# Kernel tuning notes

Hardware: AMD Instinct MI355X
Metric: run time of the kernel (lower is better)

## Reference

```python
import jax, jax.numpy as jnp
import numpy as np

N_NODES = 50000
N_EDGES = 800000
IN_DIM = 128
HIDDEN = 128
NUM_CLASSES = 64
NEG_SLOPE = 0.2


def setup_inputs() -> dict:
    key = jax.random.key(0)
    ks = jax.random.split(key, 12)
    x = jax.random.normal(ks[0], (N_NODES, IN_DIM), dtype=jnp.float32)
    src = jax.random.randint(ks[1], (N_EDGES,), 0, N_NODES, dtype=jnp.int64)
    dst = jax.random.randint(ks[2], (N_EDGES,), 0, N_NODES, dtype=jnp.int64)
    def glorot(k, shape):
        fan_in, fan_out = shape[0], shape[-1]
        s = jnp.sqrt(2.0 / (fan_in + fan_out)).astype(jnp.float32)
        return jax.random.normal(k, shape, dtype=jnp.float32) * s
    return {
        "x": x, "src": src, "dst": dst,
        # GATConv params (1 head, no bias, no residual)
        "W_gat": glorot(ks[3], (IN_DIM, HIDDEN)),
        "attn_l": glorot(ks[4], (HIDDEN,)),
        "attn_r": glorot(ks[5], (HIDDEN,)),
        # GraphConv params (norm='none', bias=True)
        "W1": glorot(ks[6], (HIDDEN, HIDDEN)),
        "b1": jnp.zeros((HIDDEN,), dtype=jnp.float32),
        "W2": glorot(ks[7], (HIDDEN, HIDDEN)),
        "b2": jnp.zeros((HIDDEN,), dtype=jnp.float32),
        "Wc": glorot(ks[8], (HIDDEN, NUM_CLASSES)),
        "bc": jnp.zeros((NUM_CLASSES,), dtype=jnp.float32),
    }


def reference(x, src, dst, W_gat, attn_l, attn_r, W1, b1, W2, b2, Wc, bc):
    N = x.shape[0]
    # --- GATConv, single head, eval mode (dropout=0) ---
    h = x @ W_gat                      # (N, H)
    el = h @ attn_l                    # (N,)
    er = h @ attn_r                    # (N,)
    e = jax.nn.leaky_relu(el[src] + er[dst], negative_slope=NEG_SLOPE)  # (E,)
    # edge softmax over incoming edges of each dst node
    emax = jax.ops.segment_max(e, dst, num_segments=N)
    ee = jnp.exp(e - emax[dst])
    esum = jax.ops.segment_sum(ee, dst, num_segments=N)
    alpha = ee / esum[dst]             # (E,) attention = reused edge weights
    h1 = jax.ops.segment_sum(h[src] * alpha[:, None], dst, num_segments=N)
    h1 = jax.nn.elu(h1)                # GATConv activation

    # --- GraphConv (norm='none') with edge_weight = alpha ---
    def gconv(hin, W, b):
        hp = hin @ W                                   # project (order is math-equivalent)
        agg = jax.ops.segment_sum(hp[src] * alpha[:, None], dst, num_segments=N)
        return agg + b

    h2 = gconv(h1, W1, b1)
    h3 = gconv(h2, W2, b2)
    logits = gconv(h3, Wc, bc)         # (N, num_classes)
    return logits
```

## Files before the change

### kernel.cpp

```cpp
#include <hip/hip_runtime.h>
#include <hip/hip_fp16.h>
#include <math.h>

#define N_NODES 50000
#define N_EDGES 800000
#define PAD_EDGES (N_EDGES + 16 * N_NODES)

typedef _Float16 half8 __attribute__((ext_vector_type(8)));
typedef float floatx16 __attribute__((ext_vector_type(16)));

#define NPREPA_BLK 129
#define NPREPP_BLK 33
#define NEDGE_BLK 3125
#define NSCAN_BLK 196

__global__ __launch_bounds__(256) void k1_prep_hist(const int* __restrict__ dst,
                                                    const float* __restrict__ Wg,
                                                    const float* __restrict__ W1,
                                                    const float* __restrict__ W2,
                                                    const float* __restrict__ b1,
                                                    int* __restrict__ deg,
                                                    int* __restrict__ rank,
                                                    __half* __restrict__ Wg_hl,
                                                    float* __restrict__ W12,
                                                    float* __restrict__ c12) {
  int b = blockIdx.x;
  if (b >= NPREPA_BLK) {
    int e = (b - NPREPA_BLK) * 256 + threadIdx.x;
    if (e < N_EDGES) rank[e] = atomicAdd(&deg[dst[e]], 1);
    return;
  }
  int e = b * 256 + threadIdx.x;
  if (e < 16384) {
    _Float16* o = (_Float16*)Wg_hl;
    int k = e >> 7, n = e & 127;
    float w = Wg[k * 128 + n];
    _Float16 hi = (_Float16)w;
    float lo = w - (float)hi;
    int oi = (((k >> 3) * 128 + n) << 3) | (k & 7);
    o[oi] = hi;
    o[16384 + oi] = (_Float16)lo;
  } else if (e < 32768) {
    int local = e - 16384;
    int k = local >> 7, n = local & 127;
    float acc = 0.f;
    for (int j = 0; j < 128; ++j) acc = fmaf(W1[k * 128 + j], W2[j * 128 + n], acc);
    W12[k * 128 + n] = acc;
  } else if (e < 32896) {
    int n = e - 32768;
    float acc = 0.f;
    for (int j = 0; j < 128; ++j) acc = fmaf(b1[j], W2[j * 128 + n], acc);
    c12[n] = acc;
  }
}

__global__ __launch_bounds__(256) void scan1_k(const int* __restrict__ deg,
                                               int* __restrict__ offs,
                                               int* __restrict__ bsum, int N) {
  __shared__ int s[256];
  int t = threadIdx.x;
  int i = blockIdx.x * 256 + t;
  int v = 0;
  if (i < N) {
    int d = deg[i];
    v = (d + 15) & ~15;
    if (v < 16) v = 16;
  }
  s[t] = v;
  __syncthreads();
  for (int o = 1; o < 256; o <<= 1) {
    int add = (t >= o) ? s[t - o] : 0;
    __syncthreads();
    s[t] += add;
    __syncthreads();
  }
  if (i < N) offs[i] = s[t] - v;
  if (t == 255) bsum[blockIdx.x] = s[255];
}

__global__ __launch_bounds__(256) void scan3_k(int* __restrict__ offs,
                                               const int* __restrict__ deg,
                                               const int* __restrict__ bsum,
                                               int N, int nb) {
  __shared__ int s[256];
  int t = threadIdx.x;
  int b = blockIdx.x;
  s[t] = (t < nb && t < b) ? bsum[t] : 0;
  __syncthreads();
  for (int o = 128; o; o >>= 1) {
    if (t < o) s[t] += s[t + o];
    __syncthreads();
  }
  int base = s[0];
  int i = b * 256 + t;
  if (i < N) {
    int o = offs[i] + base;
    offs[i] = o;
    if (i == N - 1) {
      int d = deg[i];
      int pd = (d + 15) & ~15;
      if (pd < 16) pd = 16;
      offs[N] = o + pd;
    }
  }
}

__global__ __launch_bounds__(256) void k4_prepP_scatter(const int* __restrict__ src,
                                                        const int* __restrict__ dst,
                                                        const int* __restrict__ offs,
                                                        const int* __restrict__ rank,
                                                        int* __restrict__ csr_src,
                                                        const float* __restrict__ W12,
                                                        const float* __restrict__ c12,
                                                        const float* __restrict__ Wc,
                                                        const float* __restrict__ b2,
                                                        __half* __restrict__ WPhl,
                                                        float* __restrict__ c1,
                                                        float* __restrict__ c2) {
  int b = blockIdx.x;
  if (b >= NPREPP_BLK) {
    int e = (b - NPREPP_BLK) * 256 + threadIdx.x;
    if (e < N_EDGES) csr_src[offs[dst[e]] + rank[e]] = src[e];
    return;
  }
  int e = b * 256 + threadIdx.x;
  _Float16* o = (_Float16*)WPhl;
  if (e < 8192) {
    int k = e >> 6, n = e & 63;
    float acc = 0.f;
    for (int j = 0; j < 128; ++j) acc = fmaf(W12[k * 128 + j], Wc[j * 64 + n], acc);
    _Float16 hi = (_Float16)acc;
    float lo = acc - (float)hi;
    int oi = (((k >> 3) * 64 + n) << 3) | (k & 7);
    o[oi] = hi;
    o[8192 + oi] = (_Float16)lo;
  } else if (e < 8256) {
    int n = e - 8192;
    float acc = 0.f;
    for (int j = 0; j < 128; ++j) acc = fmaf(c12[j], Wc[j * 64 + n], acc);
    c1[n] = acc;
  } else if (e < 8320) {
    int n = e - 8256;
    float acc = 0.f;
    for (int j = 0; j < 128; ++j) acc = fmaf(b2[j], Wc[j * 64 + n], acc);
    c2[n] = acc;
  }
}

template <int NCOL, bool A16, bool ELR>
__global__ __launch_bounds__(256) void mgemm_k(const void* __restrict__ Ap,
                                               const __half* __restrict__ Whl,
                                               __half* __restrict__ C16, int M,
                                               const float* __restrict__ al,
                                               const float* __restrict__ ar,
                                               float2* __restrict__ el2,
                                               float* __restrict__ er,
                                               const int* __restrict__ deg) {
  __shared__ __half Al[16][129][8];
  const int tid  = threadIdx.x;
  const int row0 = blockIdx.x * 128;
  const int lane = tid & 63;
  const int lane31 = lane & 31;
  const int q = lane >> 5;
  const int r = tid >> 6;

  if (A16) {
    const uint4* A8 = (const uint4*)Ap;
    #pragma unroll
    for (int i = 0; i < 8; ++i) {
      int idx = tid + i * 256;
      int row = idx >> 4, c = idx & 15;
      int grow = row0 + row;
      uint4 v = make_uint4(0u, 0u, 0u, 0u);
      if (grow < M) v = A8[grow * 16 + c];
      *reinterpret_cast<uint4*>(&Al[c][row][0]) = v;
    }
  } else {
    const float4* A4 = (const float4*)Ap;
    #pragma unroll
    for (int i = 0; i < 8; ++i) {
      int idx = tid + i * 256;
      int row = idx >> 4, c = idx & 15;
      int grow = row0 + row;
      half8 hv = {};
      if (grow < M) {
        float4 a0 = A4[grow * 32 + c * 2];
        float4 a1 = A4[grow * 32 + c * 2 + 1];
        hv[0] = (_Float16)a0.x; hv[1] = (_Float16)a0.y;
        hv[2] = (_Float16)a0.z; hv[3] = (_Float16)a0.w;
        hv[4] = (_Float16)a1.x; hv[5] = (_Float16)a1.y;
        hv[6] = (_Float16)a1.z; hv[7] = (_Float16)a1.w;
      }
      *reinterpret_cast<half8*>(&Al[c][row][0]) = hv;
    }
  }
  __syncthreads();

  half8 afr[8];
  #pragma unroll
  for (int s = 0; s < 8; ++s)
    afr[s] = *reinterpret_cast<const half8*>(&Al[2 * s + q][r * 32 + lane31][0]);

  const half8* B8 = reinterpret_cast<const half8*>(Whl);
  const int KN8 = 16 * NCOL;

  float elp[16], erp[16];
  if (ELR) {
    #pragma unroll
    for (int i = 0; i < 16; ++i) { elp[i] = 0.f; erp[i] = 0.f; }
  }

  #pragma unroll
  for (int tc = 0; tc < NCOL / 32; ++tc) {
    floatx16 acc = {};
    int nbase = tc * 32 + lane31;
    #pragma unroll
    for (int s = 0; s < 8; ++s) {
      int ci = (2 * s + q) * NCOL + nbase;
      half8 bl = B8[KN8 + ci];
      half8 bh = B8[ci];
      acc = __builtin_amdgcn_mfma_f32_32x32x16_f16(afr[s], bl, acc, 0, 0, 0);
      acc = __builtin_amdgcn_mfma_f32_32x32x16_f16(afr[s], bh, acc, 0, 0, 0);
    }
    if (ELR) {
      float alv = al[nbase], arv = ar[nbase];
      #pragma unroll
      for (int i = 0; i < 16; ++i) {
        elp[i] = fmaf(acc[i], alv, elp[i]);
        erp[i] = fmaf(acc[i], arv, erp[i]);
      }
    }
    #pragma unroll
    for (int i = 0; i < 16; ++i) {
      int rl = (i & 3) + 8 * (i >> 2) + 4 * q;
      int grow = row0 + r * 32 + rl;
      if (grow < M) C16[grow * NCOL + nbase] = __float2half(acc[i]);
    }
  }

  if (ELR) {
    #pragma unroll
    for (int off = 1; off <= 16; off <<= 1) {
      #pragma unroll
      for (int i = 0; i < 16; ++i) {
        elp[i] += __shfl_xor(elp[i], off);
        erp[i] += __shfl_xor(erp[i], off);
      }
    }
    if (lane31 == 0) {
      #pragma unroll
      for (int i = 0; i < 16; ++i) {
        int rl = (i & 3) + 8 * (i >> 2) + 4 * q;
        int grow = row0 + r * 32 + rl;
        if (grow < M) {
          er[grow] = erp[i];
          el2[grow] = make_float2(elp[i], (deg[grow] > 0) ? 1.f : 0.f);
        }
      }
    }
  }
}

__device__ inline void fma8(float2 acc[4], uint4 u, float a) {
  __half2* h = reinterpret_cast<__half2*>(&u);
  #pragma unroll
  for (int j = 0; j < 4; ++j) {
    float2 f = __half22float2(h[j]);
    acc[j].x = fmaf(a, f.x, acc[j].x);
    acc[j].y = fmaf(a, f.y, acc[j].y);
  }
}

__global__ __launch_bounds__(256) void aggsm_k(const int* __restrict__ offs,
                                               const int* __restrict__ deg,
                                               const int* __restrict__ csr_src,
                                               const float2* __restrict__ el2,
                                               const float* __restrict__ er,
                                               int2* __restrict__ meta,
                                               float* __restrict__ t,
                                               const __half* __restrict__ hp,
                                               __half* __restrict__ out, int N) {
  __shared__ int2 lmeta[4][64];
  int wv   = threadIdx.x >> 6;
  int w    = (blockIdx.x * 256 + threadIdx.x) >> 6;
  int lane = threadIdx.x & 63;
  if (w >= N) return;
  int o0   = offs[w];
  int pcnt = offs[w + 1] - o0;
  int cnt  = deg[w];
  int q  = lane >> 4;
  int fl = lane & 15;
  const uint4* hpq = reinterpret_cast<const uint4*>(hp);

  if (cnt <= 64) {
    bool valid = lane < cnt;
    float erv = er[w];
    int s = 0;
    float ev = -3.4e38f, flag = 0.f;
    if (valid) {
      s = csr_src[o0 + lane];
      float2 e2 = el2[s];
      float e0 = e2.x + erv;
      ev = (e0 >= 0.f) ? e0 : 0.2f * e0;
      flag = e2.y;
    }
    float m = ev;
    #pragma unroll
    for (int off = 32; off; off >>= 1) m = fmaxf(m, __shfl_xor(m, off));
    float ee = valid ? __expf(ev - m) : 0.f;
    float sum = ee, tp = ee * flag;
    #pragma unroll
    for (int off = 32; off; off >>= 1) {
      sum += __shfl_xor(sum, off);
      tp  += __shfl_xor(tp, off);
    }
    float inv = (cnt > 0) ? 1.f / sum : 0.f;
    int2 mm = make_int2(0, 0);
    if (valid) mm = make_int2(s * 16, __float_as_int(ee * inv));
    if (lane < pcnt) meta[o0 + lane] = mm;
    lmeta[wv][lane] = mm;
    if (lane == 0) t[w] = tp * inv;
  } else {
    float erv = er[w];
    float m = -3.4e38f;
    for (int i = lane; i < cnt; i += 64) {
      int s = csr_src[o0 + i];
      float2 e2 = el2[s];
      float ev = e2.x + erv;
      ev = (ev >= 0.f) ? ev : 0.2f * ev;
      m = fmaxf(m, ev);
    }
    #pragma unroll
    for (int off = 32; off; off >>= 1) m = fmaxf(m, __shfl_xor(m, off));
    float sum = 0.f, tacc = 0.f;
    int myS = 0; float myE = 0.f;
    for (int i = lane; i < cnt; i += 64) {
      int s = csr_src[o0 + i];
      float2 e2 = el2[s];
      float ev = e2.x + erv;
      ev = (ev >= 0.f) ? ev : 0.2f * ev;
      float ee = __expf(ev - m);
      meta[o0 + i] = make_int2(s * 16, __float_as_int(ee));
      sum += ee;
      tacc += ee * e2.y;
      if (i == lane) { myS = s; myE = ee; }
    }
    #pragma unroll
    for (int off = 32; off; off >>= 1) {
      sum  += __shfl_xor(sum, off);
      tacc += __shfl_xor(tacc, off);
    }
    float inv = 1.f / sum;
    if (lane == 0) t[w] = tacc * inv;
    for (int i = lane; i < cnt; i += 64) {
      int2 mm = meta[o0 + i];
      meta[o0 + i] = make_int2(mm.x, __float_as_int(__int_as_float(mm.y) * inv));
    }
    for (int i = cnt + lane; i < pcnt; i += 64) meta[o0 + i] = make_int2(0, 0);
    lmeta[wv][lane] = make_int2(myS * 16, __float_as_int(myE * inv));
  }

  float2 acc0[4] = {}, acc1[4] = {};
  int pc = pcnt < 64 ? pcnt : 64;
  int2 mA = lmeta[wv][q], mB = lmeta[wv][4 + q];
  for (int base = 8; base < pc; base += 8) {
    int2 nA = lmeta[wv][base + q], nB = lmeta[wv][base + 4 + q];
    uint4 vA = hpq[mA.x + fl], vB = hpq[mB.x + fl];
    fma8(acc0, vA, __int_as_float(mA.y));
    fma8(acc1, vB, __int_as_float(mB.y));
    mA = nA; mB = nB;
  }
  {
    uint4 vA = hpq[mA.x + fl], vB = hpq[mB.x + fl];
    fma8(acc0, vA, __int_as_float(mA.y));
    fma8(acc1, vB, __int_as_float(mB.y));
  }
  for (int p = o0 + 64 + q; p < o0 + pcnt; p += 4) {
    int2 mm = meta[p];
    fma8(acc0, hpq[mm.x + fl], __int_as_float(mm.y));
  }
  #pragma unroll
  for (int j = 0; j < 4; ++j) { acc0[j].x += acc1[j].x; acc0[j].y += acc1[j].y; }
  #pragma unroll
  for (int off = 16; off <= 32; off <<= 1) {
    #pragma unroll
    for (int j = 0; j < 4; ++j) {
      acc0[j].x += __shfl_xor(acc0[j].x, off);
      acc0[j].y += __shfl_xor(acc0[j].y, off);
    }
  }
  if (q == 0) {
    float o8[8];
    #pragma unroll
    for (int j = 0; j < 4; ++j) { o8[2 * j] = acc0[j].x; o8[2 * j + 1] = acc0[j].y; }
    #pragma unroll
    for (int j = 0; j < 8; ++j) o8[j] = (o8[j] > 0.f) ? o8[j] : (__expf(o8[j]) - 1.f);
    __half2 p0 = __floats2half2_rn(o8[0], o8[1]);
    __half2 p1 = __floats2half2_rn(o8[2], o8[3]);
    __half2 p2 = __floats2half2_rn(o8[4], o8[5]);
    __half2 p3 = __floats2half2_rn(o8[6], o8[7]);
    uint4 pk;
    pk.x = *reinterpret_cast<unsigned*>(&p0);
    pk.y = *reinterpret_cast<unsigned*>(&p1);
    pk.z = *reinterpret_cast<unsigned*>(&p2);
    pk.w = *reinterpret_cast<unsigned*>(&p3);
    *reinterpret_cast<uint4*>(&out[w * 128 + fl * 8]) = pk;
  }
}

template <bool FINAL>
__global__ __launch_bounds__(256) void agg64v_k(const int* __restrict__ offs,
                                                const int2* __restrict__ meta,
                                                const __half* __restrict__ zp,
                                                const float* __restrict__ t,
                                                const int* __restrict__ deg,
                                                const float* __restrict__ c1,
                                                const float* __restrict__ c2,
                                                const float* __restrict__ bc,
                                                void* __restrict__ outp, int N) {
  int w    = (blockIdx.x * 256 + threadIdx.x) >> 6;
  int lane = threadIdx.x & 63;
  if (w >= N) return;
  int o0 = offs[w], o1 = offs[w + 1];
  int o   = lane >> 3;
  int fl  = lane & 7;
  const uint4* hpq = reinterpret_cast<const uint4*>(zp);

  float2 acc0[4] = {}, acc1[4] = {};
  int p = o0 + o;
  int2 mA = meta[p], mB = meta[p + 8];
  for (; p + 16 < o1; p += 16) {
    int2 nA = meta[p + 16], nB = meta[p + 24];
    uint4 vA = hpq[(mA.x >> 1) + fl];
    uint4 vB = hpq[(mB.x >> 1) + fl];
    fma8(acc0, vA, __int_as_float(mA.y));
    fma8(acc1, vB, __int_as_float(mB.y));
    mA = nA; mB = nB;
  }
  {
    uint4 vA = hpq[(mA.x >> 1) + fl];
    uint4 vB = hpq[(mB.x >> 1) + fl];
    fma8(acc0, vA, __int_as_float(mA.y));
    fma8(acc1, vB, __int_as_float(mB.y));
  }
  #pragma unroll
  for (int j = 0; j < 4; ++j) { acc0[j].x += acc1[j].x; acc0[j].y += acc1[j].y; }
  #pragma unroll
  for (int off = 8; off <= 32; off <<= 1) {
    #pragma unroll
    for (int j = 0; j < 4; ++j) {
      acc0[j].x += __shfl_xor(acc0[j].x, off);
      acc0[j].y += __shfl_xor(acc0[j].y, off);
    }
  }
  if (o == 0) {
    float o8[8];
    #pragma unroll
    for (int j = 0; j < 4; ++j) { o8[2 * j] = acc0[j].x; o8[2 * j + 1] = acc0[j].y; }
    if (FINAL) {
      float tw = t[w];
      float dw = (deg[w] > 0) ? 1.f : 0.f;
      float4 a0 = reinterpret_cast<const float4*>(c1)[fl * 2];
      float4 a1 = reinterpret_cast<const float4*>(c1)[fl * 2 + 1];
      float4 d0 = reinterpret_cast<const float4*>(c2)[fl * 2];
      float4 d1 = reinterpret_cast<const float4*>(c2)[fl * 2 + 1];
      float4 b0 = reinterpret_cast<const float4*>(bc)[fl * 2];
      float4 b1v = reinterpret_cast<const float4*>(bc)[fl * 2 + 1];
      o8[0] += tw * a0.x + dw * d0.x + b0.x;
      o8[1] += tw * a0.y + dw * d0.y + b0.y;
      o8[2] += tw * a0.z + dw * d0.z + b0.z;
      o8[3] += tw * a0.w + dw * d0.w + b0.w;
      o8[4] += tw * a1.x + dw * d1.x + b1v.x;
      o8[5] += tw * a1.y + dw * d1.y + b1v.y;
      o8[6] += tw * a1.z + dw * d1.z + b1v.z;
      o8[7] += tw * a1.w + dw * d1.w + b1v.w;
      float4* of = reinterpret_cast<float4*>(outp);
      of[w * 16 + fl * 2]     = make_float4(o8[0], o8[1], o8[2], o8[3]);
      of[w * 16 + fl * 2 + 1] = make_float4(o8[4], o8[5], o8[6], o8[7]);
    } else {
      __half2 p0 = __floats2half2_rn(o8[0], o8[1]);
      __half2 p1 = __floats2half2_rn(o8[2], o8[3]);
      __half2 p2 = __floats2half2_rn(o8[4], o8[5]);
      __half2 p3 = __floats2half2_rn(o8[6], o8[7]);
      uint4 pk;
      pk.x = *reinterpret_cast<unsigned*>(&p0);
      pk.y = *reinterpret_cast<unsigned*>(&p1);
      pk.z = *reinterpret_cast<unsigned*>(&p2);
      pk.w = *reinterpret_cast<unsigned*>(&p3);
      reinterpret_cast<uint4*>(outp)[w * 8 + fl] = pk;
    }
  }
}

extern "C" void kernel_launch(void* const* d_in, const int* in_sizes, int n_in,
                              void* d_out, int out_size, void* d_ws, size_t ws_size,
                              hipStream_t stream) {
  const float* x      = (const float*)d_in[0];
  const int*   src    = (const int*)d_in[1];
  const int*   dst    = (const int*)d_in[2];
  const float* W_gat  = (const float*)d_in[3];
  const float* attn_l = (const float*)d_in[4];
  const float* attn_r = (const float*)d_in[5];
  const float* W1     = (const float*)d_in[6];
  const float* b1     = (const float*)d_in[7];
  const float* W2     = (const float*)d_in[8];
  const float* b2     = (const float*)d_in[9];
  const float* Wc     = (const float*)d_in[10];
  const float* bc     = (const float*)d_in[11];
  float* out = (float*)d_out;

  char* ws = (char*)d_ws;
  size_t off = 0;
  auto walloc = [&](size_t bytes) -> void* {
    void* p = ws + off;
    off += (bytes + 255) & ~size_t(255);
    return p;
  };
  __half* P16     = (__half*)walloc((size_t)N_NODES * 128 * 2);
  __half* F16     = (__half*)walloc((size_t)N_NODES * 128 * 2);
  float*  er      = (float*)walloc((size_t)N_NODES * 4);
  float2* el2     = (float2*)walloc((size_t)N_NODES * 8);
  float*  tbuf    = (float*)walloc((size_t)N_NODES * 4);
  int*    deg     = (int*)walloc((size_t)N_NODES * 4);
  int*    offs    = (int*)walloc((size_t)(N_NODES + 1) * 4);
  int*    rank    = (int*)walloc((size_t)N_EDGES * 4);
  int*    csr_src = (int*)walloc((size_t)PAD_EDGES * 4);
  int2*   meta    = (int2*)walloc((size_t)PAD_EDGES * 8);
  int*    bsum    = (int*)walloc(1024);
  __half* Wg_hl   = (__half*)walloc((size_t)32768 * 2);
  __half* WP_hl   = (__half*)walloc((size_t)16384 * 2);
  float*  W12     = (float*)walloc((size_t)16384 * 4);
  float*  c12     = (float*)walloc((size_t)128 * 4);
  float*  c1      = (float*)walloc((size_t)64 * 4);
  float*  c2      = (float*)walloc((size_t)64 * 4);

  hipMemsetAsync(deg, 0, (size_t)N_NODES * 4, stream);

  const dim3 blk(256);
  const int nwave_blocks = (N_NODES + 3) / 4;
  const int ngemm_blocks = (N_NODES + 127) / 128;

  k1_prep_hist<<<dim3(NPREPA_BLK + NEDGE_BLK), blk, 0, stream>>>(
      dst, W_gat, W1, W2, b1, deg, rank, Wg_hl, W12, c12);
  scan1_k<<<dim3(NSCAN_BLK), blk, 0, stream>>>(deg, offs, bsum, N_NODES);
  scan3_k<<<dim3(NSCAN_BLK), blk, 0, stream>>>(offs, deg, bsum, N_NODES, NSCAN_BLK);
  k4_prepP_scatter<<<dim3(NPREPP_BLK + NEDGE_BLK), blk, 0, stream>>>(
      src, dst, offs, rank, csr_src, W12, c12, Wc, b2, WP_hl, c1, c2);

  mgemm_k<128, false, true><<<dim3(ngemm_blocks), blk, 0, stream>>>(
      x, Wg_hl, P16, N_NODES, attn_l, attn_r, el2, er, deg);

  aggsm_k<<<dim3(nwave_blocks), blk, 0, stream>>>(offs, deg, csr_src, el2, er, meta, tbuf, P16, F16, N_NODES);
  mgemm_k<64, true, false><<<dim3(ngemm_blocks), blk, 0, stream>>>(
      F16, WP_hl, P16, N_NODES, nullptr, nullptr, nullptr, nullptr, nullptr);
  agg64v_k<false><<<dim3(nwave_blocks), blk, 0, stream>>>(offs, meta, P16, nullptr, nullptr, nullptr, nullptr, nullptr, F16, N_NODES);
  agg64v_k<false><<<dim3(nwave_blocks), blk, 0, stream>>>(offs, meta, F16, nullptr, nullptr, nullptr, nullptr, nullptr, P16, N_NODES);
  agg64v_k<true><<<dim3(nwave_blocks), blk, 0, stream>>>(offs, meta, P16, tbuf, deg, c1, c2, bc, out, N_NODES);
}
```

Measured before the change: 271.5 us.

## Fuse scan passes with decoupled lookback, shrink segment padding, specialize short-degree loops

Measured after the change: 282.0 us. +3.8%, slower.

```diff
diff --git a/kernel.cpp b/kernel.cpp
--- a/kernel.cpp
+++ b/kernel.cpp
@@ -4,7 +4,7 @@
 
 #define N_NODES 50000
 #define N_EDGES 800000
-#define PAD_EDGES (N_EDGES + 16 * N_NODES)
+#define PAD_EDGES (N_EDGES + 8 * N_NODES)
 
 typedef _Float16 half8 __attribute__((ext_vector_type(8)));
 typedef float floatx16 __attribute__((ext_vector_type(16)));
@@ -54,17 +54,51 @@
   }
 }
 
-__global__ __launch_bounds__(256) void scan1_k(const int* __restrict__ deg,
+__global__ __launch_bounds__(256) void scanP_k(const int* __restrict__ deg,
                                                int* __restrict__ offs,
-                                               int* __restrict__ bsum, int N) {
+                                               int* __restrict__ bsum,
+                                               int* __restrict__ bflag,
+                                               const float* __restrict__ W12,
+                                               const float* __restrict__ c12,
+                                               const float* __restrict__ Wc,
+                                               const float* __restrict__ b2,
+                                               __half* __restrict__ WPhl,
+                                               float* __restrict__ c1,
+                                               float* __restrict__ c2, int N) {
+  int b = blockIdx.x;
+  int t = threadIdx.x;
+  if (b >= NSCAN_BLK) {
+    int e = (b - NSCAN_BLK) * 256 + t;
+    _Float16* o = (_Float16*)WPhl;
+    if (e < 8192) {
+      int k = e >> 6, n = e & 63;
+      float acc = 0.f;
+      for (int j = 0; j < 128; ++j) acc = fmaf(W12[k * 128 + j], Wc[j * 64 + n], acc);
+      _Float16 hi = (_Float16)acc;
+      float lo = acc - (float)hi;
+      int oi = (((k >> 3) * 64 + n) << 3) | (k & 7);
+      o[oi] = hi;
+      o[8192 + oi] = (_Float16)lo;
+    } else if (e < 8256) {
+      int n = e - 8192;
+      float acc = 0.f;
+      for (int j = 0; j < 128; ++j) acc = fmaf(c12[j], Wc[j * 64 + n], acc);
+      c1[n] = acc;
+    } else if (e < 8320) {
+      int n = e - 8256;
+      float acc = 0.f;
+      for (int j = 0; j < 128; ++j) acc = fmaf(b2[j], Wc[j * 64 + n], acc);
+      c2[n] = acc;
+    }
+    return;
+  }
   __shared__ int s[256];
-  int t = threadIdx.x;
-  int i = blockIdx.x * 256 + t;
+  int i = b * 256 + t;
   int v = 0;
   if (i < N) {
     int d = deg[i];
-    v = (d + 15) & ~15;
-    if (v < 16) v = 16;
+    v = (d + 7) & ~7;
+    if (v < 8) v = 8;
   }
   s[t] = v;
   __syncthreads();
@@ -74,77 +108,44 @@
     s[t] += add;
     __syncthreads();
   }
-  if (i < N) offs[i] = s[t] - v;
-  if (t == 255) bsum[blockIdx.x] = s[255];
-}
-
-__global__ __launch_bounds__(256) void scan3_k(int* __restrict__ offs,
-                                               const int* __restrict__ deg,
-                                               const int* __restrict__ bsum,
-                                               int N, int nb) {
-  __shared__ int s[256];
-  int t = threadIdx.x;
-  int b = blockIdx.x;
-  s[t] = (t < nb && t < b) ? bsum[t] : 0;
+  int loc = s[t] - v;
+  if (t == 255) {
+    bsum[b] = s[255];
+    __hip_atomic_store(&bflag[b], 1, __ATOMIC_RELEASE, __HIP_MEMORY_SCOPE_AGENT);
+  }
+  int contrib = 0;
+  if (t < b) {
+    while (!__hip_atomic_load(&bflag[t], __ATOMIC_ACQUIRE, __HIP_MEMORY_SCOPE_AGENT))
+      __builtin_amdgcn_s_sleep(2);
+    contrib = bsum[t];
+  }
+  __syncthreads();
+  s[t] = contrib;
   __syncthreads();
   for (int o = 128; o; o >>= 1) {
     if (t < o) s[t] += s[t + o];
     __syncthreads();
   }
   int base = s[0];
-  int i = b * 256 + t;
   if (i < N) {
-    int o = offs[i] + base;
+    int o = loc + base;
     offs[i] = o;
     if (i == N - 1) {
       int d = deg[i];
-      int pd = (d + 15) & ~15;
-      if (pd < 16) pd = 16;
+      int pd = (d + 7) & ~7;
+      if (pd < 8) pd = 8;
       offs[N] = o + pd;
     }
   }
 }
 
-__global__ __launch_bounds__(256) void k4_prepP_scatter(const int* __restrict__ src,
-                                                        const int* __restrict__ dst,
-                                                        const int* __restrict__ offs,
-                                                        const int* __restrict__ rank,
-                                                        int* __restrict__ csr_src,
-                                                        const float* __restrict__ W12,
-                                                        const float* __restrict__ c12,
-                                                        const float* __restrict__ Wc,
-                                                        const float* __restrict__ b2,
-                                                        __half* __restrict__ WPhl,
-                                                        float* __restrict__ c1,
-                                                        float* __restrict__ c2) {
-  int b = blockIdx.x;
-  if (b >= NPREPP_BLK) {
-    int e = (b - NPREPP_BLK) * 256 + threadIdx.x;
-    if (e < N_EDGES) csr_src[offs[dst[e]] + rank[e]] = src[e];
-    return;
-  }
-  int e = b * 256 + threadIdx.x;
-  _Float16* o = (_Float16*)WPhl;
-  if (e < 8192) {
-    int k = e >> 6, n = e & 63;
-    float acc = 0.f;
-    for (int j = 0; j < 128; ++j) acc = fmaf(W12[k * 128 + j], Wc[j * 64 + n], acc);
-    _Float16 hi = (_Float16)acc;
-    float lo = acc - (float)hi;
-    int oi = (((k >> 3) * 64 + n) << 3) | (k & 7);
-    o[oi] = hi;
-    o[8192 + oi] = (_Float16)lo;
-  } else if (e < 8256) {
-    int n = e - 8192;
-    float acc = 0.f;
-    for (int j = 0; j < 128; ++j) acc = fmaf(c12[j], Wc[j * 64 + n], acc);
-    c1[n] = acc;
-  } else if (e < 8320) {
-    int n = e - 8256;
-    float acc = 0.f;
-    for (int j = 0; j < 128; ++j) acc = fmaf(b2[j], Wc[j * 64 + n], acc);
-    c2[n] = acc;
-  }
+__global__ __launch_bounds__(256) void scat_k(const int* __restrict__ src,
+                                              const int* __restrict__ dst,
+                                              const int* __restrict__ offs,
+                                              const int* __restrict__ rank,
+                                              int* __restrict__ csr_src) {
+  int e = blockIdx.x * 256 + threadIdx.x;
+  if (e < N_EDGES) csr_src[offs[dst[e]] + rank[e]] = src[e];
 }
 
 template <int NCOL, bool A16, bool ELR>
@@ -362,15 +363,43 @@
 
   float2 acc0[4] = {}, acc1[4] = {};
   int pc = pcnt < 64 ? pcnt : 64;
-  int2 mA = lmeta[wv][q], mB = lmeta[wv][4 + q];
-  for (int base = 8; base < pc; base += 8) {
-    int2 nA = lmeta[wv][base + q], nB = lmeta[wv][base + 4 + q];
+  int n8 = pc >> 3;
+  if (n8 == 1) {
+    int2 mA = lmeta[wv][q], mB = lmeta[wv][4 + q];
     uint4 vA = hpq[mA.x + fl], vB = hpq[mB.x + fl];
     fma8(acc0, vA, __int_as_float(mA.y));
     fma8(acc1, vB, __int_as_float(mB.y));
-    mA = nA; mB = nB;
-  }
-  {
+  } else if (n8 == 2) {
+    int2 mA0 = lmeta[wv][q],     mB0 = lmeta[wv][4 + q];
+    int2 mA1 = lmeta[wv][8 + q], mB1 = lmeta[wv][12 + q];
+    uint4 vA0 = hpq[mA0.x + fl], vB0 = hpq[mB0.x + fl];
+    uint4 vA1 = hpq[mA1.x + fl], vB1 = hpq[mB1.x + fl];
+    fma8(acc0, vA0, __int_as_float(mA0.y));
+    fma8(acc1, vB0, __int_as_float(mB0.y));
+    fma8(acc0, vA1, __int_as_float(mA1.y));
+    fma8(acc1, vB1, __int_as_float(mB1.y));
+  } else if (n8 == 3) {
+    int2 mA0 = lmeta[wv][q],      mB0 = lmeta[wv][4 + q];
+    int2 mA1 = lmeta[wv][8 + q],  mB1 = lmeta[wv][12 + q];
+    int2 mA2 = lmeta[wv][16 + q], mB2 = lmeta[wv][20 + q];
+    uint4 vA0 = hpq[mA0.x + fl], vB0 = hpq[mB0.x + fl];
+    uint4 vA1 = hpq[mA1.x + fl], vB1 = hpq[mB1.x + fl];
+    uint4 vA2 = hpq[mA2.x + fl], vB2 = hpq[mB2.x + fl];
+    fma8(acc0, vA0, __int_as_float(mA0.y));
+    fma8(acc1, vB0, __int_as_float(mB0.y));
+    fma8(acc0, vA1, __int_as_float(mA1.y));
+    fma8(acc1, vB1, __int_as_float(mB1.y));
+    fma8(acc0, vA2, __int_as_float(mA2.y));
+    fma8(acc1, vB2, __int_as_float(mB2.y));
+  } else {
+    int2 mA = lmeta[wv][q], mB = lmeta[wv][4 + q];
+    for (int base = 8; base < pc; base += 8) {
+      int2 nA = lmeta[wv][base + q], nB = lmeta[wv][base + 4 + q];
+      uint4 vA = hpq[mA.x + fl], vB = hpq[mB.x + fl];
+      fma8(acc0, vA, __int_as_float(mA.y));
+      fma8(acc1, vB, __int_as_float(mB.y));
+      mA = nA; mB = nB;
+    }
     uint4 vA = hpq[mA.x + fl], vB = hpq[mB.x + fl];
     fma8(acc0, vA, __int_as_float(mA.y));
     fma8(acc1, vB, __int_as_float(mB.y));
@@ -428,20 +457,39 @@
 
   float2 acc0[4] = {}, acc1[4] = {};
   int p = o0 + o;
-  int2 mA = meta[p], mB = meta[p + 8];
-  for (; p + 16 < o1; p += 16) {
-    int2 nA = meta[p + 16], nB = meta[p + 24];
+  int n8 = (o1 - o0) >> 3;
+  if (n8 == 1) {
+    int2 m = meta[p];
+    uint4 v = hpq[(m.x >> 1) + fl];
+    fma8(acc0, v, __int_as_float(m.y));
+  } else if (n8 == 2) {
+    int2 mA = meta[p], mB = meta[p + 8];
     uint4 vA = hpq[(mA.x >> 1) + fl];
     uint4 vB = hpq[(mB.x >> 1) + fl];
     fma8(acc0, vA, __int_as_float(mA.y));
     fma8(acc1, vB, __int_as_float(mB.y));
-    mA = nA; mB = nB;
-  }
-  {
+  } else if (n8 == 3) {
+    int2 mA = meta[p], mB = meta[p + 8], mC = meta[p + 16];
     uint4 vA = hpq[(mA.x >> 1) + fl];
     uint4 vB = hpq[(mB.x >> 1) + fl];
+    uint4 vC = hpq[(mC.x >> 1) + fl];
     fma8(acc0, vA, __int_as_float(mA.y));
     fma8(acc1, vB, __int_as_float(mB.y));
+    fma8(acc0, vC, __int_as_float(mC.y));
+  } else {
+    if (n8 & 1) {
+      int2 m = meta[p];
+      uint4 v = hpq[(m.x >> 1) + fl];
+      fma8(acc0, v, __int_as_float(m.y));
+      p += 8;
+    }
+    for (; p < o1; p += 16) {
+      int2 mA = meta[p], mB = meta[p + 8];
+      uint4 vA = hpq[(mA.x >> 1) + fl];
+      uint4 vB = hpq[(mB.x >> 1) + fl];
+      fma8(acc0, vA, __int_as_float(mA.y));
+      fma8(acc1, vB, __int_as_float(mB.y));
+    }
   }
   #pragma unroll
   for (int j = 0; j < 4; ++j) { acc0[j].x += acc1[j].x; acc0[j].y += acc1[j].y; }
@@ -521,7 +569,8 @@
   float*  er      = (float*)walloc((size_t)N_NODES * 4);
   float2* el2     = (float2*)walloc((size_t)N_NODES * 8);
   float*  tbuf    = (float*)walloc((size_t)N_NODES * 4);
-  int*    deg     = (int*)walloc((size_t)N_NODES * 4);
+  int*    deg     = (int*)walloc((size_t)N_NODES * 4 + 1024);
+  int*    bflag   = deg + N_NODES;
   int*    offs    = (int*)walloc((size_t)(N_NODES + 1) * 4);
   int*    rank    = (int*)walloc((size_t)N_EDGES * 4);
   int*    csr_src = (int*)walloc((size_t)PAD_EDGES * 4);
@@ -534,7 +583,7 @@
   float*  c1      = (float*)walloc((size_t)64 * 4);
   float*  c2      = (float*)walloc((size_t)64 * 4);
 
-  hipMemsetAsync(deg, 0, (size_t)N_NODES * 4, stream);
+  hipMemsetAsync(deg, 0, (size_t)N_NODES * 4 + 1024, stream);
 
   const dim3 blk(256);
   const int nwave_blocks = (N_NODES + 3) / 4;
@@ -542,10 +591,9 @@
 
   k1_prep_hist<<<dim3(NPREPA_BLK + NEDGE_BLK), blk, 0, stream>>>(
       dst, W_gat, W1, W2, b1, deg, rank, Wg_hl, W12, c12);
-  scan1_k<<<dim3(NSCAN_BLK), blk, 0, stream>>>(deg, offs, bsum, N_NODES);
-  scan3_k<<<dim3(NSCAN_BLK), blk, 0, stream>>>(offs, deg, bsum, N_NODES, NSCAN_BLK);
-  k4_prepP_scatter<<<dim3(NPREPP_BLK + NEDGE_BLK), blk, 0, stream>>>(
-      src, dst, offs, rank, csr_src, W12, c12, Wc, b2, WP_hl, c1, c2);
+  scanP_k<<<dim3(NSCAN_BLK + NPREPP_BLK), blk, 0, stream>>>(
+      deg, offs, bsum, bflag, W12, c12, Wc, b2, WP_hl, c1, c2, N_NODES);
+  scat_k<<<dim3(NEDGE_BLK), blk, 0, stream>>>(src, dst, offs, rank, csr_src);
 
   mgemm_k<128, false, true><<<dim3(ngemm_blocks), blk, 0, stream>>>(
       x, Wg_hl, P16, N_NODES, attn_l, attn_r, el2, er, deg);
```

## Fuse first GEMM into scan kernel and replace stored edge ranks with atomic cursors

Applied to the files above, without the earlier changes.

Result: slower. 294.7 us (+8.5%).

```diff
diff --git a/kernel.cpp b/kernel.cpp
--- a/kernel.cpp
+++ b/kernel.cpp
@@ -13,6 +13,7 @@
 #define NPREPP_BLK 33
 #define NEDGE_BLK 3125
 #define NSCAN_BLK 196
+#define NGEMM_BLK 391
 
 __global__ __launch_bounds__(256) void k1_prep_hist(const int* __restrict__ dst,
                                                     const float* __restrict__ Wg,
@@ -20,14 +21,13 @@
                                                     const float* __restrict__ W2,
                                                     const float* __restrict__ b1,
                                                     int* __restrict__ deg,
-                                                    int* __restrict__ rank,
                                                     __half* __restrict__ Wg_hl,
                                                     float* __restrict__ W12,
                                                     float* __restrict__ c12) {
   int b = blockIdx.x;
   if (b >= NPREPA_BLK) {
     int e = (b - NPREPA_BLK) * 256 + threadIdx.x;
-    if (e < N_EDGES) rank[e] = atomicAdd(&deg[dst[e]], 1);
+    if (e < N_EDGES) atomicAdd(&deg[dst[e]], 1);
     return;
   }
   int e = b * 256 + threadIdx.x;
@@ -54,17 +54,144 @@
   }
 }
 
-__global__ __launch_bounds__(256) void scan1_k(const int* __restrict__ deg,
-                                               int* __restrict__ offs,
-                                               int* __restrict__ bsum, int N) {
+template <int NCOL, bool A16, bool ELR>
+__device__ __forceinline__ void mgemm_body(int bid, const void* __restrict__ Ap,
+                                           const __half* __restrict__ Whl,
+                                           __half* __restrict__ C16, int M,
+                                           const float* __restrict__ al,
+                                           const float* __restrict__ ar,
+                                           float* __restrict__ el2x,
+                                           float* __restrict__ er) {
+  __shared__ __half Al[16][129][8];
+  const int tid  = threadIdx.x;
+  const int row0 = bid * 128;
+  const int lane = tid & 63;
+  const int lane31 = lane & 31;
+  const int q = lane >> 5;
+  const int r = tid >> 6;
+
+  if (A16) {
+    const uint4* A8 = (const uint4*)Ap;
+    #pragma unroll
+    for (int i = 0; i < 8; ++i) {
+      int idx = tid + i * 256;
+      int row = idx >> 4, c = idx & 15;
+      int grow = row0 + row;
+      uint4 v = make_uint4(0u, 0u, 0u, 0u);
+      if (grow < M) v = A8[grow * 16 + c];
+      *reinterpret_cast<uint4*>(&Al[c][row][0]) = v;
+    }
+  } else {
+    const float4* A4 = (const float4*)Ap;
+    #pragma unroll
+    for (int i = 0; i < 8; ++i) {
+      int idx = tid + i * 256;
+      int row = idx >> 4, c = idx & 15;
+      int grow = row0 + row;
+      half8 hv = {};
+      if (grow < M) {
+        float4 a0 = A4[grow * 32 + c * 2];
+        float4 a1 = A4[grow * 32 + c * 2 + 1];
+        hv[0] = (_Float16)a0.x; hv[1] = (_Float16)a0.y;
+        hv[2] = (_Float16)a0.z; hv[3] = (_Float16)a0.w;
+        hv[4] = (_Float16)a1.x; hv[5] = (_Float16)a1.y;
+        hv[6] = (_Float16)a1.z; hv[7] = (_Float16)a1.w;
+      }
+      *reinterpret_cast<half8*>(&Al[c][row][0]) = hv;
+    }
+  }
+  __syncthreads();
+
+  half8 afr[8];
+  #pragma unroll
+  for (int s = 0; s < 8; ++s)
+    afr[s] = *reinterpret_cast<const half8*>(&Al[2 * s + q][r * 32 + lane31][0]);
+
+  const half8* B8 = reinterpret_cast<const half8*>(Whl);
+  const int KN8 = 16 * NCOL;
+
+  float elp[16], erp[16];
+  if (ELR) {
+    #pragma unroll
+    for (int i = 0; i < 16; ++i) { elp[i] = 0.f; erp[i] = 0.f; }
+  }
+
+  #pragma unroll
+  for (int tc = 0; tc < NCOL / 32; ++tc) {
+    floatx16 acc = {};
+    int nbase = tc * 32 + lane31;
+    #pragma unroll
+    for (int s = 0; s < 8; ++s) {
+      int ci = (2 * s + q) * NCOL + nbase;
+      half8 bl = B8[KN8 + ci];
+      half8 bh = B8[ci];
+      acc = __builtin_amdgcn_mfma_f32_32x32x16_f16(afr[s], bl, acc, 0, 0, 0);
+      acc = __builtin_amdgcn_mfma_f32_32x32x16_f16(afr[s], bh, acc, 0, 0, 0);
+    }
+    if (ELR) {
+      float alv = al[nbase], arv = ar[nbase];
+      #pragma unroll
+      for (int i = 0; i < 16; ++i) {
+        elp[i] = fmaf(acc[i], alv, elp[i]);
+        erp[i] = fmaf(acc[i], arv, erp[i]);
+      }
+    }
+    #pragma unroll
+    for (int i = 0; i < 16; ++i) {
+      int rl = (i & 3) + 8 * (i >> 2) + 4 * q;
+      int grow = row0 + r * 32 + rl;
+      if (grow < M) C16[grow * NCOL + nbase] = __float2half(acc[i]);
+    }
+  }
+
+  if (ELR) {
+    #pragma unroll
+    for (int off = 1; off <= 16; off <<= 1) {
+      #pragma unroll
+      for (int i = 0; i < 16; ++i) {
+        elp[i] += __shfl_xor(elp[i], off);
+        erp[i] += __shfl_xor(erp[i], off);
+      }
+    }
+    if (lane31 == 0) {
+      #pragma unroll
+      for (int i = 0; i < 16; ++i) {
+        int rl = (i & 3) + 8 * (i >> 2) + 4 * q;
+        int grow = row0 + r * 32 + rl;
+        if (grow < M) {
+          er[grow] = erp[i];
+          el2x[2 * grow] = elp[i];
+        }
+      }
+    }
+  }
+}
+
+__global__ __launch_bounds__(256) void k2_scan_mgemm(const int* __restrict__ deg,
+                                                     int* __restrict__ offs,
+                                                     int* __restrict__ bsum,
+                                                     float2* __restrict__ el2,
+                                                     const float* __restrict__ x,
+                                                     const __half* __restrict__ Wg_hl,
+                                                     __half* __restrict__ P16,
+                                                     const float* __restrict__ al,
+                                                     const float* __restrict__ ar,
+                                                     float* __restrict__ er, int N) {
+  int b = blockIdx.x;
+  if (b >= NSCAN_BLK) {
+    mgemm_body<128, false, true>(b - NSCAN_BLK, x, Wg_hl, P16, N, al, ar,
+                                 reinterpret_cast<float*>(el2), er);
+    return;
+  }
   __shared__ int s[256];
   int t = threadIdx.x;
-  int i = blockIdx.x * 256 + t;
+  int i = b * 256 + t;
   int v = 0;
   if (i < N) {
     int d = deg[i];
     v = (d + 15) & ~15;
     if (v < 16) v = 16;
+    reinterpret_cast<float*>(el2)[2 * i + 1] = (d > 0) ? 1.f : 0.f;
   }
   s[t] = v;
   __syncthreads();
@@ -75,7 +202,7 @@
     __syncthreads();
   }
   if (i < N) offs[i] = s[t] - v;
-  if (t == 255) bsum[blockIdx.x] = s[255];
+  if (t == 255) bsum[b] = s[255];
 }
 
 __global__ __launch_bounds__(256) void scan3_k(int* __restrict__ offs,
@@ -108,7 +235,7 @@
 __global__ __launch_bounds__(256) void k4_prepP_scatter(const int* __restrict__ src,
                                                         const int* __restrict__ dst,
                                                         const int* __restrict__ offs,
-                                                        const int* __restrict__ rank,
+                                                        int* __restrict__ cur,
                                                         int* __restrict__ csr_src,
                                                         const float* __restrict__ W12,
                                                         const float* __restrict__ c12,
@@ -120,7 +247,11 @@
   int b = blockIdx.x;
   if (b >= NPREPP_BLK) {
     int e = (b - NPREPP_BLK) * 256 + threadIdx.x;
-    if (e < N_EDGES) csr_src[offs[dst[e]] + rank[e]] = src[e];
+    if (e < N_EDGES) {
+      int d = dst[e];
+      int r = atomicAdd(&cur[d], 1);
+      csr_src[offs[d] + r] = src[e];
+    }
     return;
   }
   int e = b * 256 + threadIdx.x;
@@ -147,118 +278,10 @@
   }
 }
 
-template <int NCOL, bool A16, bool ELR>
-__global__ __launch_bounds__(256) void mgemm_k(const void* __restrict__ Ap,
-                                               const __half* __restrict__ Whl,
-                                               __half* __restrict__ C16, int M,
-                                               const float* __restrict__ al,
-                                               const float* __restrict__ ar,
-                                               float2* __restrict__ el2,
-                                               float* __restrict__ er,
-                                               const int* __restrict__ deg) {
-  __shared__ __half Al[16][129][8];
-  const int tid  = threadIdx.x;
-  const int row0 = blockIdx.x * 128;
-  const int lane = tid & 63;
-  const int lane31 = lane & 31;
-  const int q = lane >> 5;
-  const int r = tid >> 6;
-
-  if (A16) {
-    const uint4* A8 = (const uint4*)Ap;
-    #pragma unroll
-    for (int i = 0; i < 8; ++i) {
-      int idx = tid + i * 256;
-      int row = idx >> 4, c = idx & 15;
-      int grow = row0 + row;
-      uint4 v = make_uint4(0u, 0u, 0u, 0u);
-      if (grow < M) v = A8[grow * 16 + c];
-      *reinterpret_cast<uint4*>(&Al[c][row][0]) = v;
-    }
-  } else {
-    const float4* A4 = (const float4*)Ap;
-    #pragma unroll
-    for (int i = 0; i < 8; ++i) {
-      int idx = tid + i * 256;
-      int row = idx >> 4, c = idx & 15;
-      int grow = row0 + row;
-      half8 hv = {};
-      if (grow < M) {
-        float4 a0 = A4[grow * 32 + c * 2];
-        float4 a1 = A4[grow * 32 + c * 2 + 1];
-        hv[0] = (_Float16)a0.x; hv[1] = (_Float16)a0.y;
-        hv[2] = (_Float16)a0.z; hv[3] = (_Float16)a0.w;
-        hv[4] = (_Float16)a1.x; hv[5] = (_Float16)a1.y;
-        hv[6] = (_Float16)a1.z; hv[7] = (_Float16)a1.w;
-      }
-      *reinterpret_cast<half8*>(&Al[c][row][0]) = hv;
-    }
-  }
-  __syncthreads();
-
-  half8 afr[8];
-  #pragma unroll
-  for (int s = 0; s < 8; ++s)
-    afr[s] = *reinterpret_cast<const half8*>(&Al[2 * s + q][r * 32 + lane31][0]);
-
-  const half8* B8 = reinterpret_cast<const half8*>(Whl);
-  const int KN8 = 16 * NCOL;
-
-  float elp[16], erp[16];
-  if (ELR) {
-    #pragma unroll
-    for (int i = 0; i < 16; ++i) { elp[i] = 0.f; erp[i] = 0.f; }
-  }
-
-  #pragma unroll
-  for (int tc = 0; tc < NCOL / 32; ++tc) {
-    floatx16 acc = {};
-    int nbase = tc * 32 + lane31;
-    #pragma unroll
-    for (int s = 0; s < 8; ++s) {
-      int ci = (2 * s + q) * NCOL + nbase;
-      half8 bl = B8[KN8 + ci];
-      half8 bh = B8[ci];
-      acc = __builtin_amdgcn_mfma_f32_32x32x16_f16(afr[s], bl, acc, 0, 0, 0);
-      acc = __builtin_amdgcn_mfma_f32_32x32x16_f16(afr[s], bh, acc, 0, 0, 0);
-    }
-    if (ELR) {
-      float alv = al[nbase], arv = ar[nbase];
-      #pragma unroll
-      for (int i = 0; i < 16; ++i) {
-        elp[i] = fmaf(acc[i], alv, elp[i]);
-        erp[i] = fmaf(acc[i], arv, erp[i]);
-      }
-    }
-    #pragma unroll
-    for (int i = 0; i < 16; ++i) {
-      int rl = (i & 3) + 8 * (i >> 2) + 4 * q;
-      int grow = row0 + r * 32 + rl;
-      if (grow < M) C16[grow * NCOL + nbase] = __float2half(acc[i]);
-    }
-  }
-
-  if (ELR) {
-    #pragma unroll
-    for (int off = 1; off <= 16; off <<= 1) {
-      #pragma unroll
-      for (int i = 0; i < 16; ++i) {
-        elp[i] += __shfl_xor(elp[i], off);
-        erp[i] += __shfl_xor(erp[i], off);
-      }
-    }
-    if (lane31 == 0) {
-      #pragma unroll
-      for (int i = 0; i < 16; ++i) {
-        int rl = (i & 3) + 8 * (i >> 2) + 4 * q;
-        int grow = row0 + r * 32 + rl;
-        if (grow < M) {
-          er[grow] = erp[i];
-          el2[grow] = make_float2(elp[i], (deg[grow] > 0) ? 1.f : 0.f);
-        }
-      }
-    }
-  }
+__global__ __launch_bounds__(256) void mgemm64_k(const void* __restrict__ Ap,
+                                                 const __half* __restrict__ Whl,
+                                                 __half* __restrict__ C16, int M) {
+  mgemm_body<64, true, false>(blockIdx.x, Ap, Whl, C16, M, nullptr, nullptr, nullptr, nullptr);
 }
 
 __device__ inline void fma8(float2 acc[4], uint4 u, float a) {
@@ -522,8 +545,8 @@
   float2* el2     = (float2*)walloc((size_t)N_NODES * 8);
   float*  tbuf    = (float*)walloc((size_t)N_NODES * 4);
   int*    deg     = (int*)walloc((size_t)N_NODES * 4);
+  int*    cur     = (int*)walloc((size_t)N_NODES * 4);
   int*    offs    = (int*)walloc((size_t)(N_NODES + 1) * 4);
-  int*    rank    = (int*)walloc((size_t)N_EDGES * 4);
   int*    csr_src = (int*)walloc((size_t)PAD_EDGES * 4);
   int2*   meta    = (int2*)walloc((size_t)PAD_EDGES * 8);
   int*    bsum    = (int*)walloc(1024);
@@ -534,25 +557,22 @@
   float*  c1      = (float*)walloc((size_t)64 * 4);
   float*  c2      = (float*)walloc((size_t)64 * 4);
 
-  hipMemsetAsync(deg, 0, (size_t)N_NODES * 4, stream);
+  size_t degblk = ((size_t)N_NODES * 4 + 255) & ~size_t(255);
+  hipMemsetAsync(deg, 0, degblk + (size_t)N_NODES * 4, stream);
 
   const dim3 blk(256);
   const int nwave_blocks = (N_NODES + 3) / 4;
-  const int ngemm_blocks = (N_NODES + 127) / 128;
 
   k1_prep_hist<<<dim3(NPREPA_BLK + NEDGE_BLK), blk, 0, stream>>>(
-      dst, W_gat, W1, W2, b1, deg, rank, Wg_hl, W12, c12);
-  scan1_k<<<dim3(NSCAN_BLK), blk, 0, stream>>>(deg, offs, bsum, N_NODES);
+      dst, W_gat, W1, W2, b1, deg, Wg_hl, W12, c12);
+  k2_scan_mgemm<<<dim3(NSCAN_BLK + NGEMM_BLK), blk, 0, stream>>>(
+      deg, offs, bsum, el2, x, Wg_hl, P16, attn_l, attn_r, er, N_NODES);
   scan3_k<<<dim3(NSCAN_BLK), blk, 0, stream>>>(offs, deg, bsum, N_NODES, NSCAN_BLK);
   k4_prepP_scatter<<<dim3(NPREPP_BLK + NEDGE_BLK), blk, 0, stream>>>(
-      src, dst, offs, rank, csr_src, W12, c12, Wc, b2, WP_hl, c1, c2);
-
-  mgemm_k<128, false, true><<<dim3(ngemm_blocks), blk, 0, stream>>>(
-      x, Wg_hl, P16, N_NODES, attn_l, attn_r, el2, er, deg);
+      src, dst, offs, cur, csr_src, W12, c12, Wc, b2, WP_hl, c1, c2);
 
   aggsm_k<<<dim3(nwave_blocks), blk, 0, stream>>>(offs, deg, csr_src, el2, er, meta, tbuf, P16, F16, N_NODES);
-  mgemm_k<64, true, false><<<dim3(ngemm_blocks), blk, 0, stream>>>(
-      F16, WP_hl, P16, N_NODES, nullptr, nullptr, nullptr, nullptr, nullptr);
+  mgemm64_k<<<dim3(NGEMM_BLK), blk, 0, stream>>>(F16, WP_hl, P16, N_NODES);
   agg64v_k<false><<<dim3(nwave_blocks), blk, 0, stream>>>(offs, meta, P16, nullptr, nullptr, nullptr, nullptr, nullptr, F16, N_NODES);
   agg64v_k<false><<<dim3(nwave_blocks), blk, 0, stream>>>(offs, meta, F16, nullptr, nullptr, nullptr, nullptr, nullptr, P16, N_NODES);
   agg64v_k<true><<<dim3(nwave_blocks), blk, 0, stream>>>(offs, meta, P16, tbuf, deg, c1, c2, bc, out, N_NODES);
```
